# Kernel optimization log

Hardware: AMD Instinct MI355X
Metric: run time of the kernel (lower is better)

## Reference

```python
import jax, jax.numpy as jnp
import numpy as np

EPS = 1e-6


def _att_vector(x, W, b, sharp2, th2, is_last):
    """AttentionVector on a 2D payoff slice.
    x: (N, a, m). W: (1, 2), b: (1,). Returns (N, a)."""
    # compare_param: pair (x[n,j,k], x[n,i,k]) -> Linear(2,1) -> sigmoid -> mean over k
    # Linear on the concat pair is w00*x[n,j,k] + w01*x[n,i,k] + b, so we fuse it.
    lin = W[0, 0] * x[:, None, :, :] + W[0, 1] * x[:, :, None, :] + b[0]  # (N,a,a,m)
    c = jnp.mean(jax.nn.sigmoid(lin), axis=3)  # (N,a,a)
    # max_normalize over dim 2
    c = c / (jnp.max(c, axis=2, keepdims=True) + EPS)
    # compute_player_mask
    m = jnp.mean(c, axis=2)  # (N,a)
    m = jax.nn.relu(m * sharp2[0] + th2[0])
    m = jax.nn.softmax(m, axis=1)
    if not is_last:
        m = m / (jnp.max(m, axis=1, keepdims=True) + EPS)
    return m


def setup_inputs() -> dict:
    key = jax.random.key(0)
    ks = jax.random.split(key, 16)
    N, a1, a2, f = 128, 64, 64, 2
    inp = {
        "x": jax.random.normal(ks[0], (N, f, a1, a2), dtype=jnp.float32),
        "fc_W": jax.random.normal(ks[1], (2, 2), dtype=jnp.float32) * 0.5,
        "fc_b": jax.random.normal(ks[2], (2,), dtype=jnp.float32) * 0.1,
        "p1_W": jax.random.normal(ks[3], (1, 2), dtype=jnp.float32) * 0.5,
        "p1_b": jax.random.normal(ks[4], (1,), dtype=jnp.float32) * 0.1,
        "p1_sharp": jnp.ones((1,), dtype=jnp.float32),
        "p1_th": jnp.zeros((1,), dtype=jnp.float32),
        "p2_W": jax.random.normal(ks[5], (1, 2), dtype=jnp.float32) * 0.5,
        "p2_b": jax.random.normal(ks[6], (1,), dtype=jnp.float32) * 0.1,
        "p2_sharp": jnp.ones((1,), dtype=jnp.float32),
        "p2_th": jnp.zeros((1,), dtype=jnp.float32),
        "out_W": jax.random.normal(ks[7], (1, 2), dtype=jnp.float32) * 0.5,
        "out_b": jax.random.normal(ks[8], (1,), dtype=jnp.float32) * 0.1,
        "out_sharp": jnp.ones((1,), dtype=jnp.float32),
        "out_th": jnp.zeros((1,), dtype=jnp.float32),
    }
    return inp


def reference(x, fc_W, fc_b, p1_W, p1_b, p1_sharp, p1_th,
              p2_W, p2_b, p2_sharp, p2_th,
              out_W, out_b, out_sharp, out_th):
    # x: (N, f=2, a1, a2) -> (N, a1, a2, f)
    h = jnp.transpose(x, (0, 2, 3, 1))
    # is_fc_first: Linear(2, 2) + ReLU on last dim
    h = jax.nn.relu(h @ fc_W.T + fc_b)  # (N,a1,a2,2)
    # one AttentionModule (module_layers=1, not simult)
    vec1 = _att_vector(h[..., 0], p1_W, p1_b, p1_sharp, p1_th, is_last=False)  # (N,a1)
    h = h * vec1[:, :, None, None]
    pl2 = jnp.transpose(h[..., 1], (0, 2, 1))  # (N,a2,a1)
    vec2 = _att_vector(pl2, p2_W, p2_b, p2_sharp, p2_th, is_last=False)  # (N,a2)
    h = h * vec2[:, None, :, None]
    # with_last: final AttentionVector (is_last=True) on player-1 channel
    out = _att_vector(h[..., 0], out_W, out_b, out_sharp, out_th, is_last=True)  # (N,a1)
    return out
```

## Files before the change

kernel.cpp:

```cpp
#include <hip/hip_runtime.h>


constexpr int A   = 64;
constexpr int PAD = 68;
constexpr float L2E  = 1.4426950408889634f;
constexpr float EPSF = 1e-6f;

__device__ __forceinline__ float bcast(float v, int srcLane) {
    return __int_as_float(__builtin_amdgcn_readlane(__float_as_int(v), srcLane));
}
__device__ __forceinline__ float rcpf(float v) { return __builtin_amdgcn_rcpf(v); }
__device__ __forceinline__ float ex2(float v)  { return __builtin_amdgcn_exp2f(v); }

template <int CTRL>
__device__ __forceinline__ float upd_dpp(float src) {
    return __int_as_float(__builtin_amdgcn_update_dpp(
        0, __float_as_int(src), CTRL, 0xF, 0xF, true));
}
__device__ __forceinline__ float wave_sum64(float x) {
    x += upd_dpp<0x111>(x);
    x += upd_dpp<0x112>(x);
    x += upd_dpp<0x114>(x);
    x += upd_dpp<0x118>(x);
    x += upd_dpp<0x142>(x);
    x += upd_dpp<0x143>(x);
    return bcast(x, 63);
}
__device__ __forceinline__ float wave_max64(float x) {
    x = fmaxf(x, upd_dpp<0x111>(x));
    x = fmaxf(x, upd_dpp<0x112>(x));
    x = fmaxf(x, upd_dpp<0x114>(x));
    x = fmaxf(x, upd_dpp<0x118>(x));
    x = fmaxf(x, upd_dpp<0x142>(x));
    x = fmaxf(x, upd_dpp<0x143>(x));
    return bcast(x, 63);
}

__device__ __forceinline__ void att2q(const float* __restrict__ prow,
                                      const float* __restrict__ qL,
                                      int row0, int lane,
                                      float* __restrict__ mbuf,
                                      float* __restrict__ mg)
{
    const float qreg0 = qL[row0 * PAD + lane];
    const float qreg1 = qL[(row0 + 1) * PAD + lane];
    float acc0 = 0.f, acc1 = 0.f;
#pragma unroll
    for (int c = 0; c < 4; ++c) {
        float pk[16];
        *(float4*)(&pk[0])  = *(const float4*)(prow + c * 16 + 0);
        *(float4*)(&pk[4])  = *(const float4*)(prow + c * 16 + 4);
        *(float4*)(&pk[8])  = *(const float4*)(prow + c * 16 + 8);
        *(float4*)(&pk[12]) = *(const float4*)(prow + c * 16 + 12);
#pragma unroll
        for (int g = 0; g < 4; ++g) {
            const int k = c * 16 + 4 * g;
            const float p0 = pk[4 * g], p1 = pk[4 * g + 1];
            const float p2 = pk[4 * g + 2], p3 = pk[4 * g + 3];
            {
                float u0 = fmaf(p0, bcast(qreg0, k),     1.0f);
                float u1 = fmaf(p1, bcast(qreg0, k + 1), 1.0f);
                float u2 = fmaf(p2, bcast(qreg0, k + 2), 1.0f);
                float u3 = fmaf(p3, bcast(qreg0, k + 3), 1.0f);
                float a = u0 * u1, b = u2 * u3;
                float numer = fmaf(u0 + u1, b, (u2 + u3) * a);
                acc0 = fmaf(numer, rcpf(a * b), acc0);
            }
            {
                float u0 = fmaf(p0, bcast(qreg1, k),     1.0f);
                float u1 = fmaf(p1, bcast(qreg1, k + 1), 1.0f);
                float u2 = fmaf(p2, bcast(qreg1, k + 2), 1.0f);
                float u3 = fmaf(p3, bcast(qreg1, k + 3), 1.0f);
                float a = u0 * u1, b = u2 * u3;
                float numer = fmaf(u0 + u1, b, (u2 + u3) * a);
                acc1 = fmaf(numer, rcpf(a * b), acc1);
            }
        }
    }
    const float s0 = wave_sum64(acc0), m0 = wave_max64(acc0);
    const float s1 = wave_sum64(acc1), m1 = wave_max64(acc1);
    if (lane == 0) {
        float v0 = (s0 * (1.0f / 4096.0f)) / (m0 * (1.0f / 64.0f) + EPSF);
        float v1 = (s1 * (1.0f / 4096.0f)) / (m1 * (1.0f / 64.0f) + EPSF);
        mbuf[row0]     = v0;
        mbuf[row0 + 1] = v1;
        __hip_atomic_store(mg + row0,     v0 + 2.0f, __ATOMIC_RELAXED, __HIP_MEMORY_SCOPE_AGENT);
        __hip_atomic_store(mg + row0 + 1, v1 + 2.0f, __ATOMIC_RELAXED, __HIP_MEMORY_SCOPE_AGENT);
    }
}

__device__ __forceinline__ float softmax64(float m, float sharp, float th, bool last)
{
    float v = fmaxf(0.f, m * sharp + th);
    float mx = wave_max64(v);
    float e = __expf(v - mx);
    float s = wave_sum64(e);
    float r = e / s;
    if (!last) {
        float rm = wave_max64(r);
        r = r / (rm + EPSF);
    }
    return r;
}

__device__ __forceinline__ float exch_soft(const float* __restrict__ mbuf,
                                           const float* __restrict__ mg,
                                           int half, int lane,
                                           float sharp, float th, bool last)
{
    float mv;
    if ((lane >> 5) == half) {
        mv = mbuf[lane];
    } else {
        const float* p = mg + lane;
        for (;;) {
            float f = __hip_atomic_load(p, __ATOMIC_RELAXED, __HIP_MEMORY_SCOPE_AGENT);
            unsigned u = __float_as_uint(f);
            if ((u >> 23) == 0x80u) { mv = f - 2.0f; break; }
            __builtin_amdgcn_s_sleep(1);
        }
    }
    return softmax64(mv, sharp, th, last);
}

__global__ __launch_bounds__(1024, 4)
void attn_half(const float* __restrict__ x,
               const float* __restrict__ fcW, const float* __restrict__ fcb,
               const float* __restrict__ p1W, const float* __restrict__ p1b,
               const float* __restrict__ p1s, const float* __restrict__ p1t,
               const float* __restrict__ p2W, const float* __restrict__ p2b,
               const float* __restrict__ p2s, const float* __restrict__ p2t,
               const float* __restrict__ oW,  const float* __restrict__ ob,
               const float* __restrict__ os,  const float* __restrict__ ot,
               float* __restrict__ mglob,
               float* __restrict__ out)
{
    __shared__ __align__(16) float pL[A * PAD];
    __shared__ __align__(16) float qL[A * PAD];
    __shared__ float mbuf[A];
    __shared__ float v1buf[A], v2buf[A];

    const int tid = threadIdx.x, lane = tid & 63, wv = tid >> 6;
    const int n = blockIdx.x >> 1, half = blockIdx.x & 1;
    const int row0 = half * 32 + wv * 2;
    const int i = tid >> 4, j = (tid & 15) * 4;
    float* mg = mglob + (size_t)n * 3 * A;

    const float4* x0v = (const float4*)(x + (size_t)n * 2 * A * A);
    const float4* x1v = x0v + (A * A / 4);
    const float4 a = x0v[tid];
    const float4 c = x1v[tid];
    const float w00 = fcW[0], w01 = fcW[1], w10 = fcW[2], w11 = fcW[3];
    const float b0 = fcb[0], b1 = fcb[1];
    const float h0v[4] = { fmaxf(0.f, w00 * a.x + w01 * c.x + b0),
                           fmaxf(0.f, w00 * a.y + w01 * c.y + b0),
                           fmaxf(0.f, w00 * a.z + w01 * c.z + b0),
                           fmaxf(0.f, w00 * a.w + w01 * c.w + b0) };
    const float h1v[4] = { fmaxf(0.f, w10 * a.x + w11 * c.x + b1),
                           fmaxf(0.f, w10 * a.y + w11 * c.y + b1),
                           fmaxf(0.f, w10 * a.z + w11 * c.z + b1),
                           fmaxf(0.f, w10 * a.w + w11 * c.w + b1) };

    {
        const float W0 = p1W[0], W1 = p1W[1], bb = p1b[0];
        float4 pv, qv;
        pv.x = ex2(-L2E * (W0 * h0v[0] + bb)); qv.x = ex2(-L2E * (W1 * h0v[0]));
        pv.y = ex2(-L2E * (W0 * h0v[1] + bb)); qv.y = ex2(-L2E * (W1 * h0v[1]));
        pv.z = ex2(-L2E * (W0 * h0v[2] + bb)); qv.z = ex2(-L2E * (W1 * h0v[2]));
        pv.w = ex2(-L2E * (W0 * h0v[3] + bb)); qv.w = ex2(-L2E * (W1 * h0v[3]));
        *(float4*)&pL[i * PAD + j] = pv;
        *(float4*)&qL[i * PAD + j] = qv;
    }
    __syncthreads();
    att2q(pL + lane * PAD, qL, row0, lane, mbuf, mg);
    __syncthreads();
    if (wv == 0) v1buf[lane] = exch_soft(mbuf, mg, half, lane, p1s[0], p1t[0], false);
    __syncthreads();

    {
        const float W0 = p2W[0], W1 = p2W[1], bb = p2b[0];
        const float sc = v1buf[i];
#pragma unroll
        for (int t = 0; t < 4; ++t) {
            float hv = h1v[t] * sc;
            pL[(j + t) * PAD + i] = ex2(-L2E * (W0 * hv + bb));
            qL[(j + t) * PAD + i] = ex2(-L2E * (W1 * hv));
        }
    }
    __syncthreads();
    att2q(pL + lane * PAD, qL, row0, lane, mbuf, mg + A);
    __syncthreads();
    if (wv == 0) v2buf[lane] = exch_soft(mbuf, mg + A, half, lane, p2s[0], p2t[0], false);
    __syncthreads();

    {
        const float W0 = oW[0], W1 = oW[1], bb = ob[0];
        const float sc = v1buf[i];
        const float4 v2q = *(const float4*)&v2buf[j];
        float hv0 = h0v[0] * sc * v2q.x, hv1 = h0v[1] * sc * v2q.y;
        float hv2 = h0v[2] * sc * v2q.z, hv3 = h0v[3] * sc * v2q.w;
        float4 pv, qv;
        pv.x = ex2(-L2E * (W0 * hv0 + bb)); qv.x = ex2(-L2E * (W1 * hv0));
        pv.y = ex2(-L2E * (W0 * hv1 + bb)); qv.y = ex2(-L2E * (W1 * hv1));
        pv.z = ex2(-L2E * (W0 * hv2 + bb)); qv.z = ex2(-L2E * (W1 * hv2));
        pv.w = ex2(-L2E * (W0 * hv3 + bb)); qv.w = ex2(-L2E * (W1 * hv3));
        *(float4*)&pL[i * PAD + j] = pv;
        *(float4*)&qL[i * PAD + j] = qv;
    }
    __syncthreads();
    att2q(pL + lane * PAD, qL, row0, lane, mbuf, mg + 2 * A);
    __syncthreads();

    if (wv == 0) {
        float r = exch_soft(mbuf, mg + 2 * A, half, lane, os[0], ot[0], true);
        if ((lane >> 5) == half) out[(size_t)n * A + lane] = r;
    }
}

extern "C" void kernel_launch(void* const* d_in, const int* in_sizes, int n_in,
                              void* d_out, int out_size, void* d_ws, size_t ws_size,
                              hipStream_t stream)
{
    (void)n_in; (void)out_size; (void)ws_size;
    const float* x   = (const float*)d_in[0];
    const float* fcW = (const float*)d_in[1];
    const float* fcb = (const float*)d_in[2];
    const float* p1W = (const float*)d_in[3];
    const float* p1b = (const float*)d_in[4];
    const float* p1s = (const float*)d_in[5];
    const float* p1t = (const float*)d_in[6];
    const float* p2W = (const float*)d_in[7];
    const float* p2b = (const float*)d_in[8];
    const float* p2s = (const float*)d_in[9];
    const float* p2t = (const float*)d_in[10];
    const float* oW  = (const float*)d_in[11];
    const float* ob  = (const float*)d_in[12];
    const float* os  = (const float*)d_in[13];
    const float* ot  = (const float*)d_in[14];
    float* out = (float*)d_out;

    const int N = in_sizes[0] / (2 * A * A);
    float* mglob = (float*)d_ws;

    attn_half<<<2 * N, 1024, 0, stream>>>(x, fcW, fcb,
                                          p1W, p1b, p1s, p1t,
                                          p2W, p2b, p2s, p2t,
                                          oW, ob, os, ot, mglob, out);
}
```

Before: 99.69 us.

## Split each sample across four blocks, one attention row per wave

Each sample's attention rows are now spread over four cooperating blocks instead of two. Every wave computes one row rather than two, and the blocks swap partial masks through global memory with spin-waits. This doubles the number of blocks so more CUs can work in parallel and each block finishes its compare loop sooner. In exchange, every block repeats the elementwise preprocessing and LDS fill, there is more cross-block spin traffic, and the spin-wait handshake could deadlock if not all cooperating blocks are resident at once.

```diff
diff --git a/kernel.cpp b/kernel.cpp
--- a/kernel.cpp
+++ b/kernel.cpp
@@ -36,15 +36,14 @@
     return bcast(x, 63);
 }
 
-__device__ __forceinline__ void att2q(const float* __restrict__ prow,
+__device__ __forceinline__ void att1q(const float* __restrict__ prow,
                                       const float* __restrict__ qL,
-                                      int row0, int lane,
+                                      int row, int lane,
                                       float* __restrict__ mbuf,
                                       float* __restrict__ mg)
 {
-    const float qreg0 = qL[row0 * PAD + lane];
-    const float qreg1 = qL[(row0 + 1) * PAD + lane];
-    float acc0 = 0.f, acc1 = 0.f;
+    const float qreg = qL[row * PAD + lane];
+    float acc = 0.f;
 #pragma unroll
     for (int c = 0; c < 4; ++c) {
         float pk[16];
@@ -55,37 +54,20 @@
 #pragma unroll
         for (int g = 0; g < 4; ++g) {
             const int k = c * 16 + 4 * g;
-            const float p0 = pk[4 * g], p1 = pk[4 * g + 1];
-            const float p2 = pk[4 * g + 2], p3 = pk[4 * g + 3];
-            {
-                float u0 = fmaf(p0, bcast(qreg0, k),     1.0f);
-                float u1 = fmaf(p1, bcast(qreg0, k + 1), 1.0f);
-                float u2 = fmaf(p2, bcast(qreg0, k + 2), 1.0f);
-                float u3 = fmaf(p3, bcast(qreg0, k + 3), 1.0f);
-                float a = u0 * u1, b = u2 * u3;
-                float numer = fmaf(u0 + u1, b, (u2 + u3) * a);
-                acc0 = fmaf(numer, rcpf(a * b), acc0);
-            }
-            {
-                float u0 = fmaf(p0, bcast(qreg1, k),     1.0f);
-                float u1 = fmaf(p1, bcast(qreg1, k + 1), 1.0f);
-                float u2 = fmaf(p2, bcast(qreg1, k + 2), 1.0f);
-                float u3 = fmaf(p3, bcast(qreg1, k + 3), 1.0f);
-                float a = u0 * u1, b = u2 * u3;
-                float numer = fmaf(u0 + u1, b, (u2 + u3) * a);
-                acc1 = fmaf(numer, rcpf(a * b), acc1);
-            }
+            float u0 = fmaf(pk[4 * g],     bcast(qreg, k),     1.0f);
+            float u1 = fmaf(pk[4 * g + 1], bcast(qreg, k + 1), 1.0f);
+            float u2 = fmaf(pk[4 * g + 2], bcast(qreg, k + 2), 1.0f);
+            float u3 = fmaf(pk[4 * g + 3], bcast(qreg, k + 3), 1.0f);
+            float a = u0 * u1, b = u2 * u3;
+            float numer = fmaf(u0 + u1, b, (u2 + u3) * a);
+            acc = fmaf(numer, rcpf(a * b), acc);
         }
     }
-    const float s0 = wave_sum64(acc0), m0 = wave_max64(acc0);
-    const float s1 = wave_sum64(acc1), m1 = wave_max64(acc1);
+    const float s = wave_sum64(acc), m = wave_max64(acc);
     if (lane == 0) {
-        float v0 = (s0 * (1.0f / 4096.0f)) / (m0 * (1.0f / 64.0f) + EPSF);
-        float v1 = (s1 * (1.0f / 4096.0f)) / (m1 * (1.0f / 64.0f) + EPSF);
-        mbuf[row0]     = v0;
-        mbuf[row0 + 1] = v1;
-        __hip_atomic_store(mg + row0,     v0 + 2.0f, __ATOMIC_RELAXED, __HIP_MEMORY_SCOPE_AGENT);
-        __hip_atomic_store(mg + row0 + 1, v1 + 2.0f, __ATOMIC_RELAXED, __HIP_MEMORY_SCOPE_AGENT);
+        float v = (s * (1.0f / 4096.0f)) / (m * (1.0f / 64.0f) + EPSF);
+        mbuf[row] = v;
+        __hip_atomic_store(mg + row, v + 2.0f, __ATOMIC_RELAXED, __HIP_MEMORY_SCOPE_AGENT);
     }
 }
 
@@ -105,11 +87,11 @@
 
 __device__ __forceinline__ float exch_soft(const float* __restrict__ mbuf,
                                            const float* __restrict__ mg,
-                                           int half, int lane,
+                                           int qtr, int lane,
                                            float sharp, float th, bool last)
 {
     float mv;
-    if ((lane >> 5) == half) {
+    if ((lane >> 4) == qtr) {
         mv = mbuf[lane];
     } else {
         const float* p = mg + lane;
@@ -123,17 +105,17 @@
     return softmax64(mv, sharp, th, last);
 }
 
-__global__ __launch_bounds__(1024, 4)
-void attn_half(const float* __restrict__ x,
-               const float* __restrict__ fcW, const float* __restrict__ fcb,
-               const float* __restrict__ p1W, const float* __restrict__ p1b,
-               const float* __restrict__ p1s, const float* __restrict__ p1t,
-               const float* __restrict__ p2W, const float* __restrict__ p2b,
-               const float* __restrict__ p2s, const float* __restrict__ p2t,
-               const float* __restrict__ oW,  const float* __restrict__ ob,
-               const float* __restrict__ os,  const float* __restrict__ ot,
-               float* __restrict__ mglob,
-               float* __restrict__ out)
+__global__ __launch_bounds__(1024, 8)
+void attn_qtr(const float* __restrict__ x,
+              const float* __restrict__ fcW, const float* __restrict__ fcb,
+              const float* __restrict__ p1W, const float* __restrict__ p1b,
+              const float* __restrict__ p1s, const float* __restrict__ p1t,
+              const float* __restrict__ p2W, const float* __restrict__ p2b,
+              const float* __restrict__ p2s, const float* __restrict__ p2t,
+              const float* __restrict__ oW,  const float* __restrict__ ob,
+              const float* __restrict__ os,  const float* __restrict__ ot,
+              float* __restrict__ mglob,
+              float* __restrict__ out)
 {
     __shared__ __align__(16) float pL[A * PAD];
     __shared__ __align__(16) float qL[A * PAD];
@@ -141,8 +123,8 @@
     __shared__ float v1buf[A], v2buf[A];
 
     const int tid = threadIdx.x, lane = tid & 63, wv = tid >> 6;
-    const int n = blockIdx.x >> 1, half = blockIdx.x & 1;
-    const int row0 = half * 32 + wv * 2;
+    const int n = blockIdx.x >> 2, qtr = blockIdx.x & 3;
+    const int row = qtr * 16 + wv;
     const int i = tid >> 4, j = (tid & 15) * 4;
     float* mg = mglob + (size_t)n * 3 * A;
 
@@ -172,9 +154,9 @@
         *(float4*)&qL[i * PAD + j] = qv;
     }
     __syncthreads();
-    att2q(pL + lane * PAD, qL, row0, lane, mbuf, mg);
-    __syncthreads();
-    if (wv == 0) v1buf[lane] = exch_soft(mbuf, mg, half, lane, p1s[0], p1t[0], false);
+    att1q(pL + lane * PAD, qL, row, lane, mbuf, mg);
+    __syncthreads();
+    if (wv == 0) v1buf[lane] = exch_soft(mbuf, mg, qtr, lane, p1s[0], p1t[0], false);
     __syncthreads();
 
     {
@@ -188,9 +170,9 @@
         }
     }
     __syncthreads();
-    att2q(pL + lane * PAD, qL, row0, lane, mbuf, mg + A);
-    __syncthreads();
-    if (wv == 0) v2buf[lane] = exch_soft(mbuf, mg + A, half, lane, p2s[0], p2t[0], false);
+    att1q(pL + lane * PAD, qL, row, lane, mbuf, mg + A);
+    __syncthreads();
+    if (wv == 0) v2buf[lane] = exch_soft(mbuf, mg + A, qtr, lane, p2s[0], p2t[0], false);
     __syncthreads();
 
     {
@@ -208,12 +190,12 @@
         *(float4*)&qL[i * PAD + j] = qv;
     }
     __syncthreads();
-    att2q(pL + lane * PAD, qL, row0, lane, mbuf, mg + 2 * A);
+    att1q(pL + lane * PAD, qL, row, lane, mbuf, mg + 2 * A);
     __syncthreads();
 
     if (wv == 0) {
-        float r = exch_soft(mbuf, mg + 2 * A, half, lane, os[0], ot[0], true);
-        if ((lane >> 5) == half) out[(size_t)n * A + lane] = r;
+        float r = exch_soft(mbuf, mg + 2 * A, qtr, lane, os[0], ot[0], true);
+        if ((lane >> 4) == qtr) out[(size_t)n * A + lane] = r;
     }
 }
 
@@ -242,8 +224,8 @@
     const int N = in_sizes[0] / (2 * A * A);
     float* mglob = (float*)d_ws;
 
-    attn_half<<<2 * N, 1024, 0, stream>>>(x, fcW, fcb,
-                                          p1W, p1b, p1s, p1t,
-                                          p2W, p2b, p2s, p2t,
-                                          oW, ob, os, ot, mglob, out);
-}
+    attn_qtr<<<4 * N, 1024, 0, stream>>>(x, fcW, fcb,
+                                         p1W, p1b, p1s, p1t,
+                                         p2W, p2b, p2s, p2t,
+                                         oW, ob, os, ot, mglob, out);
+}
```

New measurement: 102.0 us. 2.3% more time.
